# Performance work log

Hardware: AMD Instinct MI355X
Metric: run time of the kernel (lower is better)

Reference implementation:

```python
import jax, jax.numpy as jnp
import numpy as np
from jax import lax

N, C, S_CH = 16, 256, 512  # batch, content channels (c_in=c_out), style channels
DN = ('NCHW', 'OIHW', 'NCHW')


def setup_inputs() -> dict:
    key = jax.random.key(0)
    ks = jax.random.split(key, 8)
    p = lambda k, s: jax.random.normal(k, s, jnp.float32) * 0.05
    return {
        'style_encoding': jax.random.normal(ks[0], (N, S_CH, 4, 4), jnp.float32),
        'content_in': jax.random.normal(ks[1], (N, C, 64, 64), jnp.float32),
        # depthwise_kernel_conv: Conv2d(512, n_groups=1, kernel=2)
        'dw_w': p(ks[2], (1, S_CH, 2, 2)), 'dw_b': p(ks[3], (1,)),
        # pw_cn_kn: Conv2d(512, pointwise_groups=1, 1)
        'pw_kn_w': p(ks[4], (1, S_CH, 1, 1)), 'pw_kn_b': p(ks[5], (1,)),
        # pw_cn_bias: Conv2d(512, c_out=256, 1)
        'pw_bias_w': p(ks[6], (C, S_CH, 1, 1)), 'pw_bias_b': p(ks[7], (C,)),
    }


def reference(style_encoding, content_in, dw_w, dw_b, pw_kn_w, pw_kn_b, pw_bias_w, pw_bias_b):
    n = style_encoding.shape[0]
    # depthwise kernel prediction: (N,1,3,3) -> expand -> (N, c_out, c_in, 3, 3)
    dk = lax.conv_general_dilated(style_encoding, dw_w, (1, 1), 'VALID',
                                  dimension_numbers=DN) + dw_b[None, :, None, None]
    depthwise = jnp.broadcast_to(dk[:, None], (n, C, C, 3, 3))
    # AvgPool2d(4) on 4x4 spatial == global mean -> (N,512,1,1)
    s_d = jnp.mean(style_encoding, axis=(2, 3))  # (N,512)
    # 1x1 convs on 1x1 spatial are plain matmuls
    pw1 = s_d @ pw_kn_w[:, :, 0, 0].T + pw_kn_b              # (N,1)
    pointwise_kn = jnp.broadcast_to(pw1[:, None, :, None, None], (n, C, C, 1, 1))
    pointwise_bias = s_d @ pw_bias_w[:, :, 0, 0].T + pw_bias_b  # (N,256)
    # ReflectionPad2d((1,1,1,1))
    x = jnp.pad(content_in, ((0, 0), (0, 0), (1, 1), (1, 1)), mode='reflect')

    def sample_conv(xi, wi, pwi, bi):
        # xi: (C,H+2,W+2), wi: (C,C,3,3) dynamic per-sample weight (groups=1)
        d = lax.conv_general_dilated(xi[None], wi, (1, 1), 'VALID',
                                     dimension_numbers=DN)[0]  # (C,H,W)
        # pointwise 1x1 conv with per-sample weight + bias
        return jnp.einsum('oi,ihw->ohw', pwi[:, :, 0, 0], d) + bi[:, None, None]

    return jax.vmap(sample_conv)(x, depthwise, pointwise_kn, pointwise_bias)
```

## Files before the change

kernel.cpp:

```cpp
#include <hip/hip_runtime.h>


#define OFF_SCALE 0
#define OFF_K     16
#define OFF_SD    160
#define OFF_XS    8352

__global__ __launch_bounds__(256, 2) void ada_front(
    const float* __restrict__ style,
    const float* __restrict__ content,
    const float* __restrict__ dw_w,
    const float* __restrict__ dw_b,
    const float* __restrict__ pw_kn_w,
    const float* __restrict__ pw_kn_b,
    float* __restrict__ ws)
{
    const int t = threadIdx.x;
    __shared__ float red[4][10];
    __shared__ float4 part[8][32];

    if (blockIdx.x >= 16) {
        const int b   = blockIdx.x - 16;
        const int n   = b >> 5;
        const int sl  = b & 31;
        const int col = t & 31;
        const int g   = t >> 5;

        const float4* src = (const float4*)content
                          + ((size_t)(n * 256 + g * 32)) * 1024 + sl * 32 + col;
        float4 a = make_float4(0.f, 0.f, 0.f, 0.f);
#pragma unroll 8
        for (int c = 0; c < 32; ++c) {
            float4 v = src[(size_t)c * 1024];
            a.x += v.x; a.y += v.y; a.z += v.z; a.w += v.w;
        }
        part[g][col] = a;
        __syncthreads();
        if (g < 4) {
            float4 v = part[g + 4][col], u = part[g][col];
            part[g][col] = make_float4(u.x + v.x, u.y + v.y, u.z + v.z, u.w + v.w);
        }
        __syncthreads();
        if (g < 2) {
            float4 v = part[g + 2][col], u = part[g][col];
            part[g][col] = make_float4(u.x + v.x, u.y + v.y, u.z + v.z, u.w + v.w);
        }
        __syncthreads();
        if (g == 0) {
            float4 v = part[1][col], u = part[0][col];
            ((float4*)(ws + OFF_XS))[(size_t)n * 1024 + sl * 32 + col] =
                make_float4(u.x + v.x, u.y + v.y, u.z + v.z, u.w + v.w);
        }
        return;
    }

    const int n = blockIdx.x;

    float acc[10];
#pragma unroll
    for (int j = 0; j < 10; ++j) acc[j] = 0.f;

#pragma unroll
    for (int cc = 0; cc < 2; ++cc) {
        const int c = t + cc * 256;
        const float4* sp = (const float4*)(style + ((size_t)n * 512 + c) * 16);
        float v[16];
#pragma unroll
        for (int q = 0; q < 4; ++q) {
            float4 f = sp[q];
            v[q*4+0] = f.x; v[q*4+1] = f.y; v[q*4+2] = f.z; v[q*4+3] = f.w;
        }
        float sum = 0.f;
#pragma unroll
        for (int q = 0; q < 16; ++q) sum += v[q];
        const float sdc = sum * 0.0625f;
        ws[OFF_SD + n * 512 + c] = sdc;

        const float* w = dw_w + c * 4;
        const float w00 = w[0], w01 = w[1], w10 = w[2], w11 = w[3];
#pragma unroll
        for (int ki = 0; ki < 3; ++ki)
#pragma unroll
            for (int kj = 0; kj < 3; ++kj)
                acc[ki*3+kj] += v[ki*4 + kj]       * w00
                              + v[ki*4 + kj + 1]   * w01
                              + v[(ki+1)*4 + kj]   * w10
                              + v[(ki+1)*4 + kj+1] * w11;
        acc[9] += sdc * pw_kn_w[c];
    }

#pragma unroll
    for (int off = 32; off >= 1; off >>= 1)
#pragma unroll
        for (int j = 0; j < 10; ++j)
            acc[j] += __shfl_down(acc[j], off, 64);

    if ((t & 63) == 0) {
#pragma unroll
        for (int j = 0; j < 10; ++j) red[t >> 6][j] = acc[j];
    }
    __syncthreads();

    if (t < 10) {
        const float s = red[0][t] + red[1][t] + red[2][t] + red[3][t];
        if (t < 9) ws[OFF_K + n * 9 + t] = s + dw_b[0];
        else       ws[OFF_SCALE + n]     = 256.f * (s + pw_kn_b[0]);
    }
}

__global__ __launch_bounds__(256, 2) void ada_back(
    const float* __restrict__ ws,
    const float* __restrict__ pw_bias_w,
    const float* __restrict__ pw_bias_b,
    float4* __restrict__ out)
{
    const int bid = blockIdx.x;
    const int n   = bid >> 6;
    const int s   = bid & 63;
    const int t   = threadIdx.x;

    __shared__ float Xs[4096];
    __shared__ float bias_s[4];

    {
        const int wv = t >> 6, l = t & 63;
        const int o  = s * 4 + wv;
        const float4* wr = (const float4*)(pw_bias_w + (size_t)o * 512);
        const float4* sv = (const float4*)(ws + OFF_SD + (size_t)n * 512);
        const float4 a0 = wr[l * 2],     a1 = wr[l * 2 + 1];
        const float4 s0 = sv[l * 2],     s1 = sv[l * 2 + 1];
        float d = a0.x*s0.x + a0.y*s0.y + a0.z*s0.z + a0.w*s0.w
                + a1.x*s1.x + a1.y*s1.y + a1.z*s1.z + a1.w*s1.w;
#pragma unroll
        for (int off = 32; off >= 1; off >>= 1)
            d += __shfl_down(d, off, 64);
        if (l == 0) bias_s[wv] = d + pw_bias_b[o];
    }

    const float4* xg = (const float4*)(ws + OFF_XS) + (size_t)n * 1024;
#pragma unroll
    for (int i = 0; i < 4; ++i)
        ((float4*)Xs)[i * 256 + t] = xg[i * 256 + t];

    float k[9];
#pragma unroll
    for (int j = 0; j < 9; ++j) k[j] = ws[OFF_K + n * 9 + j];
    const float scale = ws[OFF_SCALE + n];
    __syncthreads();

    const float b0 = bias_s[0], b1 = bias_s[1], b2 = bias_s[2], b3 = bias_s[3];
    float4* obase = out + ((size_t)(n * 256 + s * 4)) * 1024;

#pragma unroll
    for (int q = 0; q < 4; ++q) {
        const int h  = q * 16 + (t >> 4);
        const int w0 = (t & 15) * 4;
        const int hm = (h == 0)  ? 1  : h - 1;
        const int hp = (h == 63) ? 62 : h + 1;
        float e0 = 0.f, e1 = 0.f, e2 = 0.f, e3 = 0.f;
        const int rows[3] = { hm, h, hp };
#pragma unroll
        for (int i = 0; i < 3; ++i) {
            const float* R = &Xs[rows[i] * 64];
            const float4 m    = *(const float4*)&R[w0];
            const float  left  = (w0 == 0)  ? R[1]  : R[w0 - 1];
            const float  right = (w0 == 60) ? R[62] : R[w0 + 4];
            const float k0 = k[i*3], k1 = k[i*3+1], k2 = k[i*3+2];
            e0 += k0*left + k1*m.x + k2*m.y;
            e1 += k0*m.x  + k1*m.y + k2*m.z;
            e2 += k0*m.y  + k1*m.z + k2*m.w;
            e3 += k0*m.z  + k1*m.w + k2*right;
        }
        e0 *= scale; e1 *= scale; e2 *= scale; e3 *= scale;

        float4* o = obase + q * 256 + t;
        o[0]    = make_float4(e0 + b0, e1 + b0, e2 + b0, e3 + b0);
        o[1024] = make_float4(e0 + b1, e1 + b1, e2 + b1, e3 + b1);
        o[2048] = make_float4(e0 + b2, e1 + b2, e2 + b2, e3 + b2);
        o[3072] = make_float4(e0 + b3, e1 + b3, e2 + b3, e3 + b3);
    }
}

extern "C" void kernel_launch(void* const* d_in, const int* in_sizes, int n_in,
                              void* d_out, int out_size, void* d_ws, size_t ws_size,
                              hipStream_t stream)
{
    const float* style     = (const float*)d_in[0];
    const float* content   = (const float*)d_in[1];
    const float* dw_w      = (const float*)d_in[2];
    const float* dw_b      = (const float*)d_in[3];
    const float* pw_kn_w   = (const float*)d_in[4];
    const float* pw_kn_b   = (const float*)d_in[5];
    const float* pw_bias_w = (const float*)d_in[6];
    const float* pw_bias_b = (const float*)d_in[7];
    float*  ws  = (float*)d_ws;
    float4* out = (float4*)d_out;

    ada_front<<<16 + 512, 256, 0, stream>>>(style, content, dw_w, dw_b,
                                            pw_kn_w, pw_kn_b, ws);
    ada_back <<<1024,     256, 0, stream>>>(ws, pw_bias_w, pw_bias_b, out);
}
```

Before: 29.98 us.

## Fuse front and back kernels into one launch with per-sample flag synchronization

Merges the two kernels into a single launch. Producer blocks (style reduction and content channel-sum) publish release flags per sample, and consumer blocks spin on acquire flags before building the output. Consumer blocks also prefetch their pw_bias weights before waiting. The aim is to remove the inter-kernel launch gap and let output blocks for one sample start while other samples are still being reduced. In exchange it adds a memset, relies on producer blocks being scheduled before consumers to avoid deadlock, and raises shared memory per block alongside a launch_bounds occupancy hint of 4.

```diff
diff --git a/kernel.cpp b/kernel.cpp
--- a/kernel.cpp
+++ b/kernel.cpp
@@ -1,26 +1,99 @@
 #include <hip/hip_runtime.h>
+#include <stdint.h>
 
 
 #define OFF_SCALE 0
 #define OFF_K     16
 #define OFF_SD    160
 #define OFF_XS    8352
-
-__global__ __launch_bounds__(256, 2) void ada_front(
+#define OFF_FLAG  73888
+#define FLAG_MAGIC 0x5F3C9A17u
+
+__global__ __launch_bounds__(256, 4) void ada_fused(
     const float* __restrict__ style,
     const float* __restrict__ content,
     const float* __restrict__ dw_w,
     const float* __restrict__ dw_b,
     const float* __restrict__ pw_kn_w,
     const float* __restrict__ pw_kn_b,
-    float* __restrict__ ws)
+    const float* __restrict__ pw_bias_w,
+    const float* __restrict__ pw_bias_b,
+    float* __restrict__ ws,
+    float4* __restrict__ out)
 {
-    const int t = threadIdx.x;
-    __shared__ float red[4][10];
+    const int bid = blockIdx.x;
+    const int t   = threadIdx.x;
+    uint32_t* flags = (uint32_t*)ws + OFF_FLAG;
+
+    __shared__ float  red[4][10];
     __shared__ float4 part[8][32];
-
-    if (blockIdx.x >= 16) {
-        const int b   = blockIdx.x - 16;
+    __shared__ float  Xs[4096];
+    __shared__ float  bias_s[4];
+
+    if (bid < 16) {
+        const int n = bid;
+
+        float acc[10];
+#pragma unroll
+        for (int j = 0; j < 10; ++j) acc[j] = 0.f;
+
+#pragma unroll
+        for (int cc = 0; cc < 2; ++cc) {
+            const int c = t + cc * 256;
+            const float4* sp = (const float4*)(style + ((size_t)n * 512 + c) * 16);
+            float v[16];
+#pragma unroll
+            for (int q = 0; q < 4; ++q) {
+                float4 f = sp[q];
+                v[q*4+0] = f.x; v[q*4+1] = f.y; v[q*4+2] = f.z; v[q*4+3] = f.w;
+            }
+            float sum = 0.f;
+#pragma unroll
+            for (int q = 0; q < 16; ++q) sum += v[q];
+            const float sdc = sum * 0.0625f;
+            ws[OFF_SD + n * 512 + c] = sdc;
+
+            const float* w = dw_w + c * 4;
+            const float w00 = w[0], w01 = w[1], w10 = w[2], w11 = w[3];
+#pragma unroll
+            for (int ki = 0; ki < 3; ++ki)
+#pragma unroll
+                for (int kj = 0; kj < 3; ++kj)
+                    acc[ki*3+kj] += v[ki*4 + kj]       * w00
+                                  + v[ki*4 + kj + 1]   * w01
+                                  + v[(ki+1)*4 + kj]   * w10
+                                  + v[(ki+1)*4 + kj+1] * w11;
+            acc[9] += sdc * pw_kn_w[c];
+        }
+
+#pragma unroll
+        for (int off = 32; off >= 1; off >>= 1)
+#pragma unroll
+            for (int j = 0; j < 10; ++j)
+                acc[j] += __shfl_down(acc[j], off, 64);
+
+        if ((t & 63) == 0) {
+#pragma unroll
+            for (int j = 0; j < 10; ++j) red[t >> 6][j] = acc[j];
+        }
+        __syncthreads();
+
+        if (t < 10) {
+            const float s = red[0][t] + red[1][t] + red[2][t] + red[3][t];
+            if (t < 9) ws[OFF_K + n * 9 + t] = s + dw_b[0];
+            else       ws[OFF_SCALE + n]     = 256.f * (s + pw_kn_b[0]);
+        }
+        __syncthreads();
+        if (t == 0) {
+            __threadfence();
+            __hip_atomic_store(&flags[n * 33 + 32], FLAG_MAGIC,
+                               __ATOMIC_RELEASE, __HIP_MEMORY_SCOPE_AGENT);
+        }
+        return;
+    }
+
+    if (bid < 528) {
+        const int b   = bid - 16;
         const int n   = b >> 5;
         const int sl  = b & 31;
         const int col = t & 31;
@@ -51,90 +124,42 @@
             ((float4*)(ws + OFF_XS))[(size_t)n * 1024 + sl * 32 + col] =
                 make_float4(u.x + v.x, u.y + v.y, u.z + v.z, u.w + v.w);
         }
+        __syncthreads();
+        if (t == 0) {
+            __threadfence();
+            __hip_atomic_store(&flags[n * 33 + sl], FLAG_MAGIC,
+                               __ATOMIC_RELEASE, __HIP_MEMORY_SCOPE_AGENT);
+        }
         return;
     }
 
-    const int n = blockIdx.x;
-
-    float acc[10];
-#pragma unroll
-    for (int j = 0; j < 10; ++j) acc[j] = 0.f;
-
-#pragma unroll
-    for (int cc = 0; cc < 2; ++cc) {
-        const int c = t + cc * 256;
-        const float4* sp = (const float4*)(style + ((size_t)n * 512 + c) * 16);
-        float v[16];
-#pragma unroll
-        for (int q = 0; q < 4; ++q) {
-            float4 f = sp[q];
-            v[q*4+0] = f.x; v[q*4+1] = f.y; v[q*4+2] = f.z; v[q*4+3] = f.w;
-        }
-        float sum = 0.f;
-#pragma unroll
-        for (int q = 0; q < 16; ++q) sum += v[q];
-        const float sdc = sum * 0.0625f;
-        ws[OFF_SD + n * 512 + c] = sdc;
-
-        const float* w = dw_w + c * 4;
-        const float w00 = w[0], w01 = w[1], w10 = w[2], w11 = w[3];
-#pragma unroll
-        for (int ki = 0; ki < 3; ++ki)
-#pragma unroll
-            for (int kj = 0; kj < 3; ++kj)
-                acc[ki*3+kj] += v[ki*4 + kj]       * w00
-                              + v[ki*4 + kj + 1]   * w01
-                              + v[(ki+1)*4 + kj]   * w10
-                              + v[(ki+1)*4 + kj+1] * w11;
-        acc[9] += sdc * pw_kn_w[c];
-    }
-
-#pragma unroll
-    for (int off = 32; off >= 1; off >>= 1)
-#pragma unroll
-        for (int j = 0; j < 10; ++j)
-            acc[j] += __shfl_down(acc[j], off, 64);
-
-    if ((t & 63) == 0) {
-#pragma unroll
-        for (int j = 0; j < 10; ++j) red[t >> 6][j] = acc[j];
+    const int c  = bid - 528;
+    const int n  = c >> 6;
+    const int s  = c & 63;
+    const int wv = t >> 6, l = t & 63;
+
+    const int o = s * 4 + wv;
+    const float4* wr = (const float4*)(pw_bias_w + (size_t)o * 512);
+    const float4 a0 = wr[l * 2], a1 = wr[l * 2 + 1];
+    const float  bb = pw_bias_b[o];
+
+    if (t < 33) {
+        while (__hip_atomic_load(&flags[n * 33 + t],
+                                 __ATOMIC_ACQUIRE, __HIP_MEMORY_SCOPE_AGENT)
+               != FLAG_MAGIC)
+            __builtin_amdgcn_s_sleep(8);
     }
     __syncthreads();
 
-    if (t < 10) {
-        const float s = red[0][t] + red[1][t] + red[2][t] + red[3][t];
-        if (t < 9) ws[OFF_K + n * 9 + t] = s + dw_b[0];
-        else       ws[OFF_SCALE + n]     = 256.f * (s + pw_kn_b[0]);
-    }
-}
-
-__global__ __launch_bounds__(256, 2) void ada_back(
-    const float* __restrict__ ws,
-    const float* __restrict__ pw_bias_w,
-    const float* __restrict__ pw_bias_b,
-    float4* __restrict__ out)
-{
-    const int bid = blockIdx.x;
-    const int n   = bid >> 6;
-    const int s   = bid & 63;
-    const int t   = threadIdx.x;
-
-    __shared__ float Xs[4096];
-    __shared__ float bias_s[4];
-
     {
-        const int wv = t >> 6, l = t & 63;
-        const int o  = s * 4 + wv;
-        const float4* wr = (const float4*)(pw_bias_w + (size_t)o * 512);
         const float4* sv = (const float4*)(ws + OFF_SD + (size_t)n * 512);
-        const float4 a0 = wr[l * 2],     a1 = wr[l * 2 + 1];
-        const float4 s0 = sv[l * 2],     s1 = sv[l * 2 + 1];
+        const float4 s0 = sv[l * 2], s1 = sv[l * 2 + 1];
         float d = a0.x*s0.x + a0.y*s0.y + a0.z*s0.z + a0.w*s0.w
                 + a1.x*s1.x + a1.y*s1.y + a1.z*s1.z + a1.w*s1.w;
 #pragma unroll
         for (int off = 32; off >= 1; off >>= 1)
             d += __shfl_down(d, off, 64);
-        if (l == 0) bias_s[wv] = d + pw_bias_b[o];
+        if (l == 0) bias_s[wv] = d + bb;
     }
 
     const float4* xg = (const float4*)(ws + OFF_XS) + (size_t)n * 1024;
@@ -173,11 +198,11 @@
         }
         e0 *= scale; e1 *= scale; e2 *= scale; e3 *= scale;
 
-        float4* o = obase + q * 256 + t;
-        o[0]    = make_float4(e0 + b0, e1 + b0, e2 + b0, e3 + b0);
-        o[1024] = make_float4(e0 + b1, e1 + b1, e2 + b1, e3 + b1);
-        o[2048] = make_float4(e0 + b2, e1 + b2, e2 + b2, e3 + b2);
-        o[3072] = make_float4(e0 + b3, e1 + b3, e2 + b3, e3 + b3);
+        float4* ob = obase + q * 256 + t;
+        ob[0]    = make_float4(e0 + b0, e1 + b0, e2 + b0, e3 + b0);
+        ob[1024] = make_float4(e0 + b1, e1 + b1, e2 + b1, e3 + b1);
+        ob[2048] = make_float4(e0 + b2, e1 + b2, e2 + b2, e3 + b2);
+        ob[3072] = make_float4(e0 + b3, e1 + b3, e2 + b3, e3 + b3);
     }
 }
 
@@ -196,7 +221,9 @@
     float*  ws  = (float*)d_ws;
     float4* out = (float4*)d_out;
 
-    ada_front<<<16 + 512, 256, 0, stream>>>(style, content, dw_w, dw_b,
-                                            pw_kn_w, pw_kn_b, ws);
-    ada_back <<<1024,     256, 0, stream>>>(ws, pw_bias_w, pw_bias_b, out);
+    hipMemsetAsync((char*)d_ws + (size_t)OFF_FLAG * 4, 0, 16 * 33 * 4, stream);
+
+    ada_fused<<<1552, 256, 0, stream>>>(style, content, dw_w, dw_b,
+                                        pw_kn_w, pw_kn_b,
+                                        pw_bias_w, pw_bias_b, ws, out);
 }
```

New measurement: 97.60 us. +225.5%, slower.
